# Kernel tuning notes

Measured on AMD Instinct MI355X. Metric: run time of the kernel, lower is better.

Reference implementation:

```python
import jax, jax.numpy as jnp
import numpy as np

B, S, D, NB = 8, 8192, 512, 16


def _ln(x, g, b, eps=1e-5):
    m = jnp.mean(x, axis=-1, keepdims=True)
    v = jnp.var(x, axis=-1, keepdims=True)
    return (x - m) / jnp.sqrt(v + eps) * g + b


def setup_inputs() -> dict:
    key = jax.random.key(0)
    ks = jax.random.split(key, 12)
    s = 0.02
    f32 = jnp.float32
    return {
        "emb_input": jax.random.normal(ks[0], (B, S, D), f32),
        "dis_input": jax.random.normal(ks[1], (B, S, D), f32),
        "torsion": jax.random.normal(ks[2], (B, D), f32),
        "dis_unlocked": 1,
        "delay_steps": 3,
        # embodied selector + per-block params (stacked over NB blocks)
        "emb_sel_W": jax.random.normal(ks[3], (D, NB), f32) * s,
        "emb_sel_b": jnp.zeros((NB,), f32),
        "emb_ln_g": jnp.ones((NB, D), f32),
        "emb_ln_b": jnp.zeros((NB, D), f32),
        "emb_w1": jax.random.normal(ks[4], (NB, D, D), f32) * s,
        "emb_b1": jnp.zeros((NB, D), f32),
        "emb_w2": jax.random.normal(ks[5], (NB, D, D), f32) * s,
        "emb_b2": jnp.zeros((NB, D), f32),
        # disembodied selector + per-block params
        "dis_sel_W": jax.random.normal(ks[6], (D, NB), f32) * s,
        "dis_sel_b": jnp.zeros((NB,), f32),
        "dis_ln1_g": jnp.ones((NB, D), f32),
        "dis_ln1_b": jnp.zeros((NB, D), f32),
        "dis_attn_W": jax.random.normal(ks[7], (NB, D, D), f32) * s,
        "dis_attn_b": jnp.zeros((NB, D), f32),
        "dis_ln2_g": jnp.ones((NB, D), f32),
        "dis_ln2_b": jnp.zeros((NB, D), f32),
        "dis_ff1_W": jax.random.normal(ks[8], (NB, D, 2 * D), f32) * s,
        "dis_ff1_b": jnp.zeros((NB, 2 * D), f32),
        "dis_ff2_W": jax.random.normal(ks[9], (NB, 2 * D, D), f32) * s,
        "dis_ff2_b": jnp.zeros((NB, D), f32),
    }


def reference(emb_input, dis_input, torsion, dis_unlocked, delay_steps,
              emb_sel_W, emb_sel_b, emb_ln_g, emb_ln_b, emb_w1, emb_b1, emb_w2, emb_b2,
              dis_sel_W, dis_sel_b, dis_ln1_g, dis_ln1_b, dis_attn_W, dis_attn_b,
              dis_ln2_g, dis_ln2_b, dis_ff1_W, dis_ff1_b, dis_ff2_W, dis_ff2_b):
    # ---- embodied branch: sigmoid-gated top-2 routing (indices from batch elem 0)
    scores = jax.nn.sigmoid(jnp.mean(emb_input, axis=1) @ emb_sel_W + emb_sel_b)  # [B,NB]
    _, top = jax.lax.top_k(scores[0], 2)
    t_emb = 1.0 + torsion[:, None, :] * 0.1  # [B,1,D]
    h = emb_input
    for i in range(2):  # fixed top-2, unrolled; block params gathered dynamically
        idx = top[i]
        hn = _ln(h, emb_ln_g[idx], emb_ln_b[idx])
        hn = jnp.tanh(hn @ emb_w1[idx] + emb_b1[idx]) @ emb_w2[idx] + emb_b2[idx]
        h = h + hn * t_emb * 0.3
    emb_h = h

    # ---- disembodied branch (dis_unlocked is a static Python int)
    dis_h = None
    if dis_unlocked:
        delayed = jnp.mean(dis_input, axis=1)  # [B,D]; single-write buffer returns current mean
        dscores = jax.nn.sigmoid(delayed @ dis_sel_W + dis_sel_b)
        _, dtop = jax.lax.top_k(dscores[0], 2)
        t_dis = 1.0 + torsion[:, None, :] * 0.05
        dh = dis_input
        for i in range(2):
            idx = dtop[i]
            h1 = _ln(dh, dis_ln1_g[idx], dis_ln1_b[idx])
            h1 = h1 @ dis_attn_W[idx] + dis_attn_b[idx]
            h1 = (h1 + delayed[:, None, :] * 0.2) * t_dis
            hm = dh + h1 * 0.5
            h2 = _ln(hm, dis_ln2_g[idx], dis_ln2_b[idx])
            h2 = jax.nn.gelu(h2 @ dis_ff1_W[idx] + dis_ff1_b[idx], approximate=False)
            h2 = h2 @ dis_ff2_W[idx] + dis_ff2_b[idx]
            dh = hm + h2 * 0.5
        dis_h = dh
    return (emb_h, dis_h)
```

## Files before the change

### kernel.cpp

```cpp
#include <hip/hip_runtime.h>
#include <stdint.h>

#define B_  8
#define S_  8192
#define D_  512
#define NB_ 16
#define M_  (B_*S_)

typedef short bf16x8 __attribute__((ext_vector_type(8)));
typedef float f32x4  __attribute__((ext_vector_type(4)));

static __device__ __forceinline__ unsigned short f2bf(float f) {
  unsigned int u = __float_as_uint(f);
  u += 0x7fff + ((u >> 16) & 1);
  return (unsigned short)(u >> 16);
}

static __device__ __forceinline__ void async_copy16(const unsigned short* g,
                                                    unsigned short* l) {
  auto* g1 = reinterpret_cast<const __attribute__((address_space(1))) uint32_t*>(
      reinterpret_cast<uintptr_t>(g));
  auto* l3 = reinterpret_cast<__attribute__((address_space(3))) uint32_t*>(
      reinterpret_cast<uintptr_t>(l));
  __builtin_amdgcn_global_load_lds(g1, l3, 16, 0, 0);
}

__global__ __launch_bounds__(256) void zero_kernel(float* p, int n) {
  int i = blockIdx.x * 256 + threadIdx.x;
  if (i < n) p[i] = 0.f;
}

__global__ __launch_bounds__(512) void colmean_kernel(const float* __restrict__ x,
                                                      float* __restrict__ acc) {
  int b = blockIdx.x, d = threadIdx.x;
  const float* p = x + ((size_t)b * S_ + (size_t)blockIdx.y * 512) * D_ + d;
  float s = 0.f;
  #pragma unroll 8
  for (int i = 0; i < 512; i++) s += p[(size_t)i * D_];
  atomicAdd(&acc[b * D_ + d], s);
}

__global__ __launch_bounds__(128) void top2_kernel(const float* __restrict__ embAcc,
                                                   const float* __restrict__ embW,
                                                   const float* __restrict__ embB,
                                                   const float* __restrict__ disAcc,
                                                   const float* __restrict__ disW,
                                                   const float* __restrict__ disB,
                                                   int* __restrict__ out) {
  int wave = threadIdx.x >> 6, lane = threadIdx.x & 63;
  const float* acc = wave ? disAcc : embAcc;
  const float* W   = wave ? disW   : embW;
  const float* bb  = wave ? disB   : embB;
  const float invS = 1.f / (float)S_;
  float logit[NB_];
  for (int nb = 0; nb < NB_; nb++) {
    float s = 0.f;
    for (int d = lane; d < D_; d += 64) s += acc[d] * invS * W[d * NB_ + nb];
    for (int o = 32; o; o >>= 1) s += __shfl_xor(s, o);
    logit[nb] = s + bb[nb];
  }
  if (lane == 0) {
    int i0 = 0;
    for (int i = 1; i < NB_; i++) if (logit[i] > logit[i0]) i0 = i;
    int i1 = (i0 == 0) ? 1 : 0;
    for (int i = 0; i < NB_; i++) if (i != i0 && logit[i] > logit[i1]) i1 = i;
    out[wave * 2 + 0] = i0;
    out[wave * 2 + 1] = i1;
  }
}

__global__ __launch_bounds__(256) void ln_cast_kernel(const float* __restrict__ x,
                                                      const float* __restrict__ gB,
                                                      const float* __restrict__ bB,
                                                      const int* __restrict__ idxPtr,
                                                      unsigned short* __restrict__ out) {
  int row  = blockIdx.x * 4 + (threadIdx.x >> 6);
  int lane = threadIdx.x & 63;
  const float4* xr = (const float4*)(x + (size_t)row * D_ + lane * 8);
  float4 v0 = xr[0], v1 = xr[1];
  float s  = v0.x + v0.y + v0.z + v0.w + v1.x + v1.y + v1.z + v1.w;
  float sq = v0.x*v0.x + v0.y*v0.y + v0.z*v0.z + v0.w*v0.w
           + v1.x*v1.x + v1.y*v1.y + v1.z*v1.z + v1.w*v1.w;
  for (int o = 32; o; o >>= 1) { s += __shfl_xor(s, o); sq += __shfl_xor(sq, o); }
  float mean = s * (1.f / D_);
  float var  = sq * (1.f / D_) - mean * mean;
  float rstd = rsqrtf(var + 1e-5f);
  int idx = *idxPtr;
  const float4* g4 = (const float4*)(gB + (size_t)idx * D_ + lane * 8);
  const float4* b4 = (const float4*)(bB + (size_t)idx * D_ + lane * 8);
  float4 g0 = g4[0], g1 = g4[1], c0 = b4[0], c1 = b4[1];
  float xv[8] = {v0.x, v0.y, v0.z, v0.w, v1.x, v1.y, v1.z, v1.w};
  float gv[8] = {g0.x, g0.y, g0.z, g0.w, g1.x, g1.y, g1.z, g1.w};
  float bv[8] = {c0.x, c0.y, c0.z, c0.w, c1.x, c1.y, c1.z, c1.w};
  unsigned short o8[8] __attribute__((aligned(16)));
  #pragma unroll
  for (int k = 0; k < 8; k++) o8[k] = f2bf((xv[k] - mean) * rstd * gv[k] + bv[k]);
  *(uint4*)(out + (size_t)row * D_ + lane * 8) = *(const uint4*)o8;
}

__global__ __launch_bounds__(256) void wconvert_kernel(const float* __restrict__ srcAll,
                                                       const int* __restrict__ idxPtr,
                                                       int K, int N,
                                                       unsigned short* __restrict__ dst) {
  __shared__ float t[32][33];
  int idx = *idxPtr;
  const float* src = srcAll + (size_t)idx * K * N;
  int k0 = blockIdx.y * 32, n0 = blockIdx.x * 32;
  int tid = threadIdx.x;
  int kl = tid >> 5, nl = tid & 31;
  #pragma unroll
  for (int r = 0; r < 4; r++)
    t[kl + r * 8][nl] = src[(size_t)(k0 + kl + r * 8) * N + n0 + nl];
  __syncthreads();
  #pragma unroll
  for (int r = 0; r < 4; r++)
    dst[(size_t)(n0 + kl + r * 8) * K + k0 + nl] = f2bf(t[nl][kl + r * 8]);
}

template<int EPI>
__global__ __launch_bounds__(512, 2) void gemm_kernel(const unsigned short* __restrict__ A,
                                                      const unsigned short* __restrict__ Bt,
                                                      int K, int N,
                                                      const int* __restrict__ idxPtr,
                                                      const float* __restrict__ biasBase,
                                                      const float* __restrict__ hin,
                                                      float* __restrict__ fout,
                                                      unsigned short* __restrict__ bout,
                                                      const float* __restrict__ torsion,
                                                      const float* __restrict__ dAcc) {
  __shared__ __align__(16) unsigned short lds[4][2][8192];
  const int tid  = threadIdx.x;
  const int wid  = tid >> 6, lane = tid & 63;
  const int quad = lane >> 4, l16 = lane & 15;
  const int wr = wid >> 2, wc = wid & 3;

  const int nT  = N >> 8;
  const int lgn = (nT == 2) ? 1 : 2;
  const int perX = gridDim.x >> 3;
  const int tile = ((int)blockIdx.x & 7) * perX + ((int)blockIdx.x >> 3);
  const int m0 = (tile >> lgn) << 8;
  const int n0 = (tile & (nT - 1)) << 8;

  const int srow = tid >> 2;
  const int scol = (((tid & 3) ^ ((tid >> 3) & 3)) * 8);
  const unsigned short* Ag0 = A  + (size_t)(m0 + srow) * K + scol;
  const unsigned short* Ag1 = Ag0 + (size_t)128 * K;
  const unsigned short* Bg0 = Bt + (size_t)(n0 + srow) * K + scol;
  const unsigned short* Bg1 = Bg0 + (size_t)128 * K;

  auto stageA = [&](int kt, int b) {
    async_copy16(Ag0 + (size_t)kt * 32, &lds[b][0][tid * 8]);
    async_copy16(Ag1 + (size_t)kt * 32, &lds[b][0][4096 + tid * 8]);
  };
  auto stageB = [&](int kt, int b) {
    async_copy16(Bg0 + (size_t)kt * 32, &lds[b][1][tid * 8]);
    async_copy16(Bg1 + (size_t)kt * 32, &lds[b][1][4096 + tid * 8]);
  };

  f32x4 acc[8][4] = {};
  const int nK = K >> 5;

  stageA(0, 0); stageB(0, 0);
  stageA(1, 1); stageB(1, 1);
  stageA(2, 2); stageB(2, 2);

  const int rsw  = (l16 >> 1) & 3;
  const int aoff = (wr * 128 + l16) * 32 + ((quad ^ rsw) * 8);
  const int boff = (wc * 64  + l16) * 32 + ((quad ^ rsw) * 8);

  for (int k = 0; k < nK; ++k) {
    const int cur = k & 3;
    const int nxt = (k + 3) & 3;
    const int kn  = (k + 3 < nK) ? (k + 3) : 0;
    stageA(kn, nxt);
    asm volatile("s_waitcnt vmcnt(10)" ::: "memory");
    asm volatile("s_barrier" ::: "memory");

    const unsigned short* Ab = &lds[cur][0][aoff];
    const unsigned short* Bb = &lds[cur][1][boff];
    bf16x8 af[4], bfr[4];
    #pragma unroll
    for (int i = 0; i < 4; ++i) af[i]  = *(const bf16x8*)(Ab + i * 512);
    #pragma unroll
    for (int j = 0; j < 4; ++j) bfr[j] = *(const bf16x8*)(Bb + j * 512);
    __builtin_amdgcn_s_setprio(1);
    #pragma unroll
    for (int i = 0; i < 4; ++i)
      #pragma unroll
      for (int j = 0; j < 4; ++j)
        acc[i][j] = __builtin_amdgcn_mfma_f32_16x16x32_bf16(af[i], bfr[j], acc[i][j], 0, 0, 0);
    __builtin_amdgcn_s_setprio(0);

    stageB(kn, nxt);
    #pragma unroll
    for (int i = 0; i < 4; ++i) af[i] = *(const bf16x8*)(Ab + (64 + i * 16) * 32);
    __builtin_amdgcn_s_setprio(1);
    #pragma unroll
    for (int i = 0; i < 4; ++i)
      #pragma unroll
      for (int j = 0; j < 4; ++j)
        acc[4 + i][j] = __builtin_amdgcn_mfma_f32_16x16x32_bf16(af[i], bfr[j], acc[4 + i][j], 0, 0, 0);
    __builtin_amdgcn_s_setprio(0);
    asm volatile("s_barrier" ::: "memory");
  }

  const int idx = *idxPtr;
  const float* bias = biasBase + (size_t)idx * N;
  const float invS = 1.f / (float)S_;
  #pragma unroll
  for (int mf = 0; mf < 8; ++mf) {
    int rowb = m0 + wr * 128 + mf * 16 + quad * 4;
    #pragma unroll
    for (int nf = 0; nf < 4; ++nf) {
      int col = n0 + wc * 64 + nf * 16 + l16;
      float bc = bias[col];
      #pragma unroll
      for (int r = 0; r < 4; ++r) {
        int row = rowb + r;
        size_t off = (size_t)row * N + col;
        float v = acc[mf][nf][r] + bc;
        if constexpr (EPI == 0) {
          bout[off] = f2bf(tanhf(v));
        } else if constexpr (EPI == 1) {
          int b = row >> 13;
          float t = 1.f + 0.1f * torsion[b * D_ + col];
          fout[off] = hin[off] + v * t * 0.3f;
        } else if constexpr (EPI == 2) {
          int b = row >> 13;
          float t = 1.f + 0.05f * torsion[b * D_ + col];
          float h1 = (v + 0.2f * dAcc[b * D_ + col] * invS) * t;
          fout[off] = hin[off] + 0.5f * h1;
        } else if constexpr (EPI == 3) {
          float gl = 0.5f * v * (1.f + erff(v * 0.70710678118654752f));
          bout[off] = f2bf(gl);
        } else {
          fout[off] = hin[off] + 0.5f * v;
        }
      }
    }
  }
  asm volatile("s_waitcnt vmcnt(0)" ::: "memory");
}

extern "C" void kernel_launch(void* const* d_in, const int* in_sizes, int n_in,
                              void* d_out, int out_size, void* d_ws, size_t ws_size,
                              hipStream_t stream) {
  const float* emb_input  = (const float*)d_in[0];
  const float* dis_input  = (const float*)d_in[1];
  const float* torsion    = (const float*)d_in[2];
  const float* emb_sel_W  = (const float*)d_in[5];
  const float* emb_sel_b  = (const float*)d_in[6];
  const float* emb_ln_g   = (const float*)d_in[7];
  const float* emb_ln_b   = (const float*)d_in[8];
  const float* emb_w1     = (const float*)d_in[9];
  const float* emb_b1     = (const float*)d_in[10];
  const float* emb_w2     = (const float*)d_in[11];
  const float* emb_b2     = (const float*)d_in[12];
  const float* dis_sel_W  = (const float*)d_in[13];
  const float* dis_sel_b  = (const float*)d_in[14];
  const float* dis_ln1_g  = (const float*)d_in[15];
  const float* dis_ln1_b  = (const float*)d_in[16];
  const float* dis_attn_W = (const float*)d_in[17];
  const float* dis_attn_b = (const float*)d_in[18];
  const float* dis_ln2_g  = (const float*)d_in[19];
  const float* dis_ln2_b  = (const float*)d_in[20];
  const float* dis_ff1_W  = (const float*)d_in[21];
  const float* dis_ff1_b  = (const float*)d_in[22];
  const float* dis_ff2_W  = (const float*)d_in[23];
  const float* dis_ff2_b  = (const float*)d_in[24];

  char* w = (char*)d_ws;
  float* accE = (float*)w;
  float* accD = (float*)(w + 16384);
  int*   top  = (int*)(w + 32768);
  size_t o = 33024;
  unsigned short* w1t   = (unsigned short*)(w + o); o += 524288;
  unsigned short* w2t   = (unsigned short*)(w + o); o += 524288;
  unsigned short* attnT = (unsigned short*)(w + o); o += 524288;
  unsigned short* ff1T  = (unsigned short*)(w + o); o += 1048576;
  unsigned short* ff2T  = (unsigned short*)(w + o); o += 1048576;
  unsigned short* Abuf  = (unsigned short*)(w + o); o += (size_t)M_ * D_ * 2;
  unsigned short* T1    = (unsigned short*)(w + o); o += (size_t)M_ * D_ * 2;

  float* outEmb = (float*)d_out;
  float* outDis = outEmb + (size_t)M_ * D_;
  unsigned short* Gbuf = (unsigned short*)d_out;

  zero_kernel<<<32, 256, 0, stream>>>(accE, 2 * B_ * D_);
  colmean_kernel<<<dim3(1, 16), 512, 0, stream>>>(emb_input, accE);
  colmean_kernel<<<dim3(8, 16), 512, 0, stream>>>(dis_input, accD);
  top2_kernel<<<1, 128, 0, stream>>>(accE, emb_sel_W, emb_sel_b,
                                     accD, dis_sel_W, dis_sel_b, top);

  for (int s = 0; s < 2; s++) {
    const int* di = top + 2 + s;
    const float* dh = (s == 0) ? dis_input : outDis;
    wconvert_kernel<<<dim3(16, 16), 256, 0, stream>>>(dis_attn_W, di, 512, 512, attnT);
    wconvert_kernel<<<dim3(32, 16), 256, 0, stream>>>(dis_ff1_W,  di, 512, 1024, ff1T);
    wconvert_kernel<<<dim3(16, 32), 256, 0, stream>>>(dis_ff2_W,  di, 1024, 512, ff2T);
    ln_cast_kernel<<<M_ / 4, 256, 0, stream>>>(dh, dis_ln1_g, dis_ln1_b, di, Abuf);
    gemm_kernel<2><<<512, 512, 0, stream>>>(Abuf, attnT, 512, 512, di,
        dis_attn_b, dh, outDis, nullptr, torsion, accD);
    ln_cast_kernel<<<M_ / 4, 256, 0, stream>>>(outDis, dis_ln2_g, dis_ln2_b, di, Abuf);
    gemm_kernel<3><<<1024, 512, 0, stream>>>(Abuf, ff1T, 512, 1024, di,
        dis_ff1_b, nullptr, nullptr, Gbuf, nullptr, nullptr);
    gemm_kernel<4><<<512, 512, 0, stream>>>(Gbuf, ff2T, 1024, 512, di,
        dis_ff2_b, outDis, outDis, nullptr, nullptr, nullptr);
  }

  for (int s = 0; s < 2; s++) {
    const int* ei = top + s;
    const float* h = (s == 0) ? emb_input : outEmb;
    wconvert_kernel<<<dim3(16, 16), 256, 0, stream>>>(emb_w1, ei, 512, 512, w1t);
    wconvert_kernel<<<dim3(16, 16), 256, 0, stream>>>(emb_w2, ei, 512, 512, w2t);
    ln_cast_kernel<<<M_ / 4, 256, 0, stream>>>(h, emb_ln_g, emb_ln_b, ei, Abuf);
    gemm_kernel<0><<<512, 512, 0, stream>>>(Abuf, w1t, 512, 512, ei,
        emb_b1, nullptr, nullptr, T1, nullptr, nullptr);
    gemm_kernel<1><<<512, 512, 0, stream>>>(T1, w2t, 512, 512, ei,
        emb_b2, h, outEmb, nullptr, torsion, nullptr);
  }
}
```

Baseline: 1.638 ms.

## Fuse following LayerNorm into residual GEMM epilogues via full-row tiles

Adds a GEMM variant whose tiles are 128 rows by the full 512 output columns. The residual epilogue can then compute per-row mean and variance through shuffles and shared memory and write the next LayerNorm's bf16 input directly. Four of the six standalone ln_cast passes are dropped, which removes a full fp32 read and bf16 write of the activations per fused boundary. The cost is a different tiling with a 3-stage ring, more accumulator registers, fewer column-parallel tiles, and a one-pass E[x²]−mean² variance that can lose precision.

```diff
diff --git a/kernel.cpp b/kernel.cpp
--- a/kernel.cpp
+++ b/kernel.cpp
@@ -123,11 +123,7 @@
                                                       int K, int N,
                                                       const int* __restrict__ idxPtr,
                                                       const float* __restrict__ biasBase,
-                                                      const float* __restrict__ hin,
-                                                      float* __restrict__ fout,
-                                                      unsigned short* __restrict__ bout,
-                                                      const float* __restrict__ torsion,
-                                                      const float* __restrict__ dAcc) {
+                                                      unsigned short* __restrict__ bout) {
   __shared__ __align__(16) unsigned short lds[4][2][8192];
   const int tid  = threadIdx.x;
   const int wid  = tid >> 6, lane = tid & 63;
@@ -206,7 +202,6 @@
 
   const int idx = *idxPtr;
   const float* bias = biasBase + (size_t)idx * N;
-  const float invS = 1.f / (float)S_;
   #pragma unroll
   for (int mf = 0; mf < 8; ++mf) {
     int rowb = m0 + wr * 128 + mf * 16 + quad * 4;
@@ -216,25 +211,163 @@
       float bc = bias[col];
       #pragma unroll
       for (int r = 0; r < 4; ++r) {
-        int row = rowb + r;
-        size_t off = (size_t)row * N + col;
+        size_t off = (size_t)(rowb + r) * N + col;
         float v = acc[mf][nf][r] + bc;
         if constexpr (EPI == 0) {
           bout[off] = f2bf(tanhf(v));
-        } else if constexpr (EPI == 1) {
-          int b = row >> 13;
-          float t = 1.f + 0.1f * torsion[b * D_ + col];
-          fout[off] = hin[off] + v * t * 0.3f;
-        } else if constexpr (EPI == 2) {
-          int b = row >> 13;
-          float t = 1.f + 0.05f * torsion[b * D_ + col];
-          float h1 = (v + 0.2f * dAcc[b * D_ + col] * invS) * t;
-          fout[off] = hin[off] + 0.5f * h1;
-        } else if constexpr (EPI == 3) {
+        } else {
           float gl = 0.5f * v * (1.f + erff(v * 0.70710678118654752f));
           bout[off] = f2bf(gl);
+        }
+      }
+    }
+  }
+  asm volatile("s_waitcnt vmcnt(0)" ::: "memory");
+}
+
+template<int EPI, bool DO_LN>
+__global__ __launch_bounds__(512, 2) void gemm_ln_kernel(const unsigned short* __restrict__ A,
+                                                         const unsigned short* __restrict__ Bt,
+                                                         int K,
+                                                         const int* __restrict__ idxPtr,
+                                                         const float* __restrict__ biasBase,
+                                                         const float* __restrict__ hin,
+                                                         float* __restrict__ fout,
+                                                         const float* __restrict__ torsion,
+                                                         const float* __restrict__ dAcc,
+                                                         const float* __restrict__ lnG,
+                                                         const float* __restrict__ lnB,
+                                                         const int* __restrict__ lnIdxPtr,
+                                                         unsigned short* __restrict__ aout) {
+  __shared__ __align__(16) unsigned short ring[3][20480];
+  __shared__ float psum[128][4];
+  __shared__ float psq[128][4];
+  const int tid  = threadIdx.x;
+  const int wid  = tid >> 6, lane = tid & 63;
+  const int quad = lane >> 4, l16 = lane & 15;
+  const int wr = wid >> 2, wc = wid & 3;
+
+  const int perX = gridDim.x >> 3;
+  const int tile = ((int)blockIdx.x & 7) * perX + ((int)blockIdx.x >> 3);
+  const int m0 = tile << 7;
+
+  const int srow = tid >> 2;
+  const int scol = (((tid & 3) ^ ((tid >> 3) & 3)) * 8);
+  const unsigned short* Ag = A  + (size_t)(m0 + srow) * K + scol;
+  const unsigned short* Bg = Bt + (size_t)srow * K + scol;
+
+  auto stage = [&](int kt, int slot) {
+    unsigned short* base = &ring[slot][0];
+    async_copy16(Ag + (size_t)kt * 32, base + tid * 8);
+    #pragma unroll
+    for (int j = 0; j < 4; ++j)
+      async_copy16(Bg + (size_t)(j * 128) * K + (size_t)kt * 32,
+                   base + 4096 + j * 4096 + tid * 8);
+  };
+
+  f32x4 acc[4][8] = {};
+  const int nK = K >> 5;
+
+  stage(0, 0);
+  stage(1, 1);
+
+  const int rsw  = (l16 >> 1) & 3;
+  const int aoff = (wr * 64  + l16) * 32 + ((quad ^ rsw) * 8);
+  const int boff = 4096 + (wc * 128 + l16) * 32 + ((quad ^ rsw) * 8);
+
+  for (int k = 0; k < nK; ++k) {
+    const int cur = k % 3;
+    const int nxt = (k + 2) % 3;
+    const int kn  = (k + 2 < nK) ? (k + 2) : 0;
+    stage(kn, nxt);
+    asm volatile("s_waitcnt vmcnt(10)" ::: "memory");
+    asm volatile("s_barrier" ::: "memory");
+
+    const unsigned short* Ab = &ring[cur][aoff];
+    const unsigned short* Bb = &ring[cur][boff];
+    bf16x8 af[4], bfr[8];
+    #pragma unroll
+    for (int i = 0; i < 4; ++i) af[i]  = *(const bf16x8*)(Ab + i * 512);
+    #pragma unroll
+    for (int j = 0; j < 8; ++j) bfr[j] = *(const bf16x8*)(Bb + j * 512);
+    __builtin_amdgcn_s_setprio(1);
+    #pragma unroll
+    for (int i = 0; i < 4; ++i)
+      #pragma unroll
+      for (int j = 0; j < 8; ++j)
+        acc[i][j] = __builtin_amdgcn_mfma_f32_16x16x32_bf16(af[i], bfr[j], acc[i][j], 0, 0, 0);
+    __builtin_amdgcn_s_setprio(0);
+    asm volatile("s_barrier" ::: "memory");
+  }
+
+  const int idx = *idxPtr;
+  const float* bias = biasBase + (size_t)idx * 512;
+  const int bcn = m0 >> 13;
+  const float invS = 1.f / (float)S_;
+  float bc[8], tv[8], dv[8];
+  #pragma unroll
+  for (int nf = 0; nf < 8; ++nf) {
+    int col = wc * 128 + nf * 16 + l16;
+    bc[nf] = bias[col];
+    if constexpr (EPI == 1) tv[nf] = 1.f + 0.1f  * torsion[bcn * D_ + col];
+    if constexpr (EPI == 2) tv[nf] = 1.f + 0.05f * torsion[bcn * D_ + col];
+    if constexpr (EPI == 2) dv[nf] = 0.2f * dAcc[bcn * D_ + col] * invS;
+  }
+  #pragma unroll
+  for (int mf = 0; mf < 4; ++mf) {
+    #pragma unroll
+    for (int r = 0; r < 4; ++r) {
+      int rowl = wr * 64 + mf * 16 + quad * 4 + r;
+      size_t rbase = (size_t)(m0 + rowl) * 512;
+      float s = 0.f, sq = 0.f;
+      #pragma unroll
+      for (int nf = 0; nf < 8; ++nf) {
+        int col = wc * 128 + nf * 16 + l16;
+        float v = acc[mf][nf][r] + bc[nf];
+        float res;
+        if constexpr (EPI == 1) {
+          res = hin[rbase + col] + v * tv[nf] * 0.3f;
+        } else if constexpr (EPI == 2) {
+          res = hin[rbase + col] + 0.5f * ((v + dv[nf]) * tv[nf]);
         } else {
-          fout[off] = hin[off] + 0.5f * v;
+          res = hin[rbase + col] + 0.5f * v;
+        }
+        fout[rbase + col] = res;
+        acc[mf][nf][r] = res;
+        s += res; sq += res * res;
+      }
+      if constexpr (DO_LN) {
+        #pragma unroll
+        for (int o = 1; o < 16; o <<= 1) { s += __shfl_xor(s, o); sq += __shfl_xor(sq, o); }
+        if (l16 == 0) { psum[rowl][wc] = s; psq[rowl][wc] = sq; }
+      }
+    }
+  }
+  if constexpr (DO_LN) {
+    __syncthreads();
+    const int li = *lnIdxPtr;
+    float gv[8], bv[8];
+    #pragma unroll
+    for (int nf = 0; nf < 8; ++nf) {
+      int col = wc * 128 + nf * 16 + l16;
+      gv[nf] = lnG[(size_t)li * D_ + col];
+      bv[nf] = lnB[(size_t)li * D_ + col];
+    }
+    #pragma unroll
+    for (int mf = 0; mf < 4; ++mf) {
+      #pragma unroll
+      for (int r = 0; r < 4; ++r) {
+        int rowl = wr * 64 + mf * 16 + quad * 4 + r;
+        float ms = psum[rowl][0] + psum[rowl][1] + psum[rowl][2] + psum[rowl][3];
+        float mq = psq[rowl][0]  + psq[rowl][1]  + psq[rowl][2]  + psq[rowl][3];
+        float mean = ms * (1.f / D_);
+        float var  = mq * (1.f / D_) - mean * mean;
+        float rstd = rsqrtf(var + 1e-5f);
+        size_t rbase = (size_t)(m0 + rowl) * 512;
+        #pragma unroll
+        for (int nf = 0; nf < 8; ++nf) {
+          int col = wc * 128 + nf * 16 + l16;
+          aout[rbase + col] = f2bf((acc[mf][nf][r] - mean) * rstd * gv[nf] + bv[nf]);
         }
       }
     }
@@ -286,37 +419,42 @@
   float* outDis = outEmb + (size_t)M_ * D_;
   unsigned short* Gbuf = (unsigned short*)d_out;
 
+  const int* di0 = top + 2; const int* di1 = top + 3;
+  const int* ei0 = top + 0; const int* ei1 = top + 1;
+
   zero_kernel<<<32, 256, 0, stream>>>(accE, 2 * B_ * D_);
   colmean_kernel<<<dim3(1, 16), 512, 0, stream>>>(emb_input, accE);
   colmean_kernel<<<dim3(8, 16), 512, 0, stream>>>(dis_input, accD);
   top2_kernel<<<1, 128, 0, stream>>>(accE, emb_sel_W, emb_sel_b,
                                      accD, dis_sel_W, dis_sel_b, top);
 
-  for (int s = 0; s < 2; s++) {
-    const int* di = top + 2 + s;
-    const float* dh = (s == 0) ? dis_input : outDis;
-    wconvert_kernel<<<dim3(16, 16), 256, 0, stream>>>(dis_attn_W, di, 512, 512, attnT);
-    wconvert_kernel<<<dim3(32, 16), 256, 0, stream>>>(dis_ff1_W,  di, 512, 1024, ff1T);
-    wconvert_kernel<<<dim3(16, 32), 256, 0, stream>>>(dis_ff2_W,  di, 1024, 512, ff2T);
-    ln_cast_kernel<<<M_ / 4, 256, 0, stream>>>(dh, dis_ln1_g, dis_ln1_b, di, Abuf);
-    gemm_kernel<2><<<512, 512, 0, stream>>>(Abuf, attnT, 512, 512, di,
-        dis_attn_b, dh, outDis, nullptr, torsion, accD);
-    ln_cast_kernel<<<M_ / 4, 256, 0, stream>>>(outDis, dis_ln2_g, dis_ln2_b, di, Abuf);
-    gemm_kernel<3><<<1024, 512, 0, stream>>>(Abuf, ff1T, 512, 1024, di,
-        dis_ff1_b, nullptr, nullptr, Gbuf, nullptr, nullptr);
-    gemm_kernel<4><<<512, 512, 0, stream>>>(Gbuf, ff2T, 1024, 512, di,
-        dis_ff2_b, outDis, outDis, nullptr, nullptr, nullptr);
-  }
-
-  for (int s = 0; s < 2; s++) {
-    const int* ei = top + s;
-    const float* h = (s == 0) ? emb_input : outEmb;
-    wconvert_kernel<<<dim3(16, 16), 256, 0, stream>>>(emb_w1, ei, 512, 512, w1t);
-    wconvert_kernel<<<dim3(16, 16), 256, 0, stream>>>(emb_w2, ei, 512, 512, w2t);
-    ln_cast_kernel<<<M_ / 4, 256, 0, stream>>>(h, emb_ln_g, emb_ln_b, ei, Abuf);
-    gemm_kernel<0><<<512, 512, 0, stream>>>(Abuf, w1t, 512, 512, ei,
-        emb_b1, nullptr, nullptr, T1, nullptr, nullptr);
-    gemm_kernel<1><<<512, 512, 0, stream>>>(T1, w2t, 512, 512, ei,
-        emb_b2, h, outEmb, nullptr, torsion, nullptr);
-  }
-}
+  wconvert_kernel<<<dim3(16, 16), 256, 0, stream>>>(dis_attn_W, di0, 512, 512, attnT);
+  wconvert_kernel<<<dim3(32, 16), 256, 0, stream>>>(dis_ff1_W,  di0, 512, 1024, ff1T);
+  wconvert_kernel<<<dim3(16, 32), 256, 0, stream>>>(dis_ff2_W,  di0, 1024, 512, ff2T);
+  ln_cast_kernel<<<M_ / 4, 256, 0, stream>>>(dis_input, dis_ln1_g, dis_ln1_b, di0, Abuf);
+  gemm_ln_kernel<2, true><<<512, 512, 0, stream>>>(Abuf, attnT, 512, di0, dis_attn_b,
+      dis_input, outDis, torsion, accD, dis_ln2_g, dis_ln2_b, di0, T1);
+  gemm_kernel<3><<<1024, 512, 0, stream>>>(T1, ff1T, 512, 1024, di0, dis_ff1_b, Gbuf);
+  gemm_ln_kernel<4, true><<<512, 512, 0, stream>>>(Gbuf, ff2T, 1024, di0, dis_ff2_b,
+      outDis, outDis, nullptr, nullptr, dis_ln1_g, dis_ln1_b, di1, Abuf);
+  wconvert_kernel<<<dim3(16, 16), 256, 0, stream>>>(dis_attn_W, di1, 512, 512, attnT);
+  wconvert_kernel<<<dim3(32, 16), 256, 0, stream>>>(dis_ff1_W,  di1, 512, 1024, ff1T);
+  wconvert_kernel<<<dim3(16, 32), 256, 0, stream>>>(dis_ff2_W,  di1, 1024, 512, ff2T);
+  gemm_ln_kernel<2, true><<<512, 512, 0, stream>>>(Abuf, attnT, 512, di1, dis_attn_b,
+      outDis, outDis, torsion, accD, dis_ln2_g, dis_ln2_b, di1, T1);
+  gemm_kernel<3><<<1024, 512, 0, stream>>>(T1, ff1T, 512, 1024, di1, dis_ff1_b, Gbuf);
+  gemm_ln_kernel<4, false><<<512, 512, 0, stream>>>(Gbuf, ff2T, 1024, di1, dis_ff2_b,
+      outDis, outDis, nullptr, nullptr, nullptr, nullptr, nullptr, nullptr);
+
+  wconvert_kernel<<<dim3(16, 16), 256, 0, stream>>>(emb_w1, ei0, 512, 512, w1t);
+  wconvert_kernel<<<dim3(16, 16), 256, 0, stream>>>(emb_w2, ei0, 512, 512, w2t);
+  ln_cast_kernel<<<M_ / 4, 256, 0, stream>>>(emb_input, emb_ln_g, emb_ln_b, ei0, Abuf);
+  gemm_kernel<0><<<512, 512, 0, stream>>>(Abuf, w1t, 512, 512, ei0, emb_b1, T1);
+  gemm_ln_kernel<1, true><<<512, 512, 0, stream>>>(T1, w2t, 512, ei0, emb_b2,
+      emb_input, outEmb, torsion, nullptr, emb_ln_g, emb_ln_b, ei1, Abuf);
+  wconvert_kernel<<<dim3(16, 16), 256, 0, stream>>>(emb_w1, ei1, 512, 512, w1t);
+  wconvert_kernel<<<dim3(16, 16), 256, 0, stream>>>(emb_w2, ei1, 512, 512, w2t);
+  gemm_kernel<0><<<512, 512, 0, stream>>>(Abuf, w1t, 512, 512, ei1, emb_b1, T1);
+  gemm_ln_kernel<1, false><<<512, 512, 0, stream>>>(T1, w2t, 512, ei1, emb_b2,
+      outEmb, outEmb, torsion, nullptr, nullptr, nullptr, nullptr, nullptr);
+}
```

After: 2.037 ms. +24.3%, slower.
